# Kernel optimization log

Hardware: AMD Instinct MI355X
Metric: run time of the kernel (lower is better)

Reference implementation:

```python
import jax, jax.numpy as jnp
import numpy as np

# dims: batch, d_features(m), n_subsets, sub_size(k=ceil(m/n)), heads, d_k, d_v, conv kernel, d_out
B, M, N, K, H, DK, DV, KER, D = 512, 4096, 64, 64, 8, 32, 4, 3, 4096
DOUT_PER = D // N  # d_out_per_subset = 64
EPS_LN = 1e-5      # torch nn.LayerNorm default eps


def setup_inputs() -> dict:
    key = jax.random.key(0)
    ks = jax.random.split(key, 8)
    s = 0.02  # xavier-like scale
    return {
        "features": jax.random.normal(ks[0], (B, M), dtype=jnp.float32),
        # per-head permutation of the m feature indices (f_shuffle(m, h, seeds))
        "shuffled_index": jnp.argsort(jax.random.uniform(ks[1], (H, M)), axis=1).astype(jnp.int32),
        "gamma": jnp.ones((M,), jnp.float32),
        "beta": jnp.zeros((M,), jnp.float32),
        "W_q": (jax.random.normal(ks[2], (H * DK, K)) * s).astype(jnp.float32),   # Linear(k, h*d_k)
        "W_k": (jax.random.normal(ks[3], (H, DK, K)) * s).astype(jnp.float32),    # grouped Conv1d(h, h*d_k, kernel=k, stride=k)
        "W_v1": (jax.random.normal(ks[4], (H, DV, KER)) * s).astype(jnp.float32), # grouped Conv1d(h, h*d_v, kernel)
        "W_v2": (jax.random.normal(ks[5], (H, DV)) * s).astype(jnp.float32),      # grouped Conv1d(h*d_v, h, 1)
        "W_fc": (jax.random.normal(ks[6], (DOUT_PER, H * K)) * s).astype(jnp.float32),
    }


def reference(features, shuffled_index, gamma, beta, W_q, W_k, W_v1, W_v2, W_fc):
    b = features.shape[0]
    # LayerNorm over m (query path only)
    mu = features.mean(-1, keepdims=True)
    var = ((features - mu) ** 2).mean(-1, keepdims=True)
    q_in = (features - mu) / jnp.sqrt(var + EPS_LN) * gamma + beta

    # shuffled gather: [b, H, M]  (k*n == m here so k_pad/q_pad are no-ops)
    sf = features[:, shuffled_index]

    # query: [b, n, k] -> Linear(k, h*d_k) -> [b, H, N, DK]
    q = jnp.einsum('bnk,ek->bne', q_in.reshape(b, N, K), W_q)
    q = q.reshape(b, N, H, DK).transpose(0, 2, 1, 3)

    # key: grouped conv kernel=stride=k == per-subset contraction -> [b, H, DK, N]
    kf = sf.reshape(b, H, N, K)
    key_ = jnp.einsum('bhnk,hdk->bhdn', kf, W_k)

    # value: [b, N, H, K], right-pad by KER-1, depthwise conv -> relu -> 1x1 conv -> +residual
    v = kf.transpose(0, 2, 1, 3)  # [b, N, H, K]
    vp = jnp.pad(v, ((0, 0), (0, 0), (0, 0), (0, KER - 1)))
    win = jnp.stack([vp[..., t:t + K] for t in range(KER)], axis=-1)  # [b,N,H,K,KER]
    v1 = jnp.einsum('bnhpt,hdt->bnhdp', win, W_v1)
    v2 = jnp.einsum('bnhdp,hd->bnhp', jax.nn.relu(v1), W_v2)
    v = (v2 + v).transpose(0, 2, 1, 3)  # [b, H, N, K]

    # scaled dot-product attention, temperature = sqrt(m)
    attn = jax.nn.softmax(jnp.einsum('bhqd,bhdk->bhqk', q, key_) / jnp.sqrt(jnp.float32(M)), axis=-1)
    out = jnp.einsum('bhqk,bhks->bhqs', attn, v)           # [b, H, N, K]
    out = out.transpose(0, 2, 1, 3).reshape(b, N, H * K)   # [b, N, H*K]
    out = jnp.einsum('bnf,of->bno', out, W_fc).reshape(b, N * DOUT_PER)
    return out, attn.reshape(b * H, N, N)
```

## Files before the change

### kernel.cpp

```cpp
#include <hip/hip_runtime.h>

typedef __bf16 v8bf __attribute__((ext_vector_type(8)));
typedef __bf16 v4bf __attribute__((ext_vector_type(4)));
typedef __bf16 v2bf __attribute__((ext_vector_type(2)));
typedef float  v4f  __attribute__((ext_vector_type(4)));
typedef float  v2f  __attribute__((ext_vector_type(2)));
typedef unsigned long long u64;

namespace {

constexpr int kB = 512, kM = 4096, kH = 8;


__global__ __launch_bounds__(256) void k0_weights(
    const float* __restrict__ Wq, const float* __restrict__ Wk,
    const float* __restrict__ Wfc,
    __bf16* __restrict__ wq, __bf16* __restrict__ wk, __bf16* __restrict__ wfc,
    float* __restrict__ out) {
  int i = blockIdx.x * 256 + threadIdx.x;
  float4 z = make_float4(0.f, 0.f, 0.f, 0.f);
#pragma unroll
  for (int j = 0; j < 4; ++j) reinterpret_cast<float4*>(out)[i + j * 131072] = z;
  if (i < 16384) {
    int e = i >> 6, k = i & 63;
    int dst = ((e >> 4) * 2 + (k >> 5)) * 512 + (e & 15) * 32 + (k & 31);
    wq[dst] = (__bf16)(Wq[i] * 0.015625f);
  } else if (i < 32768) {
    int j = i - 16384;
    int e = j >> 6, k = j & 63;
    int dst = ((e >> 4) * 2 + (k >> 5)) * 512 + (e & 15) * 32 + (k & 31);
    wk[dst] = (__bf16)Wk[j];
  } else if (i < 65536) {
    int j = i - 32768;
    int o = j >> 9, f = j & 511;
    int dst = ((o >> 4) * 16 + (f >> 5)) * 512 + (o & 15) * 32 + (f & 31);
    wfc[dst] = (__bf16)Wfc[j];
  }
}

__global__ __launch_bounds__(256, 4) void k_fused(
    const float* __restrict__ feat, const int* __restrict__ sidx,
    const float* __restrict__ gamma, const float* __restrict__ beta,
    const __bf16* __restrict__ wq, const __bf16* __restrict__ wk,
    const float* __restrict__ Wv1, const float* __restrict__ Wv2,
    const __bf16* __restrict__ wfc, float* __restrict__ out) {
  __shared__ __align__(16) __bf16 smem[18432];
  __shared__ float red[4];
  __bf16* s_feat = smem;
  __bf16* s_kf   = smem + 4096;
  __bf16* s_K0   = smem + 8704;
  __bf16* s_K1   = smem + 11264;
  __bf16* s_vT   = smem + 13824;
  __bf16* s_qin  = smem + 4096;

  const int b = blockIdx.x, half = blockIdx.y, h0 = 4 * half;
  const int t = threadIdx.x, w = t >> 6, lane = t & 63;
  const int quad = lane >> 4, l16 = lane & 15;
  const int myrow = 16 * w + l16;

  const float4* frow4 = reinterpret_cast<const float4*>(feat + (size_t)b * kM);
  const float4* g4  = reinterpret_cast<const float4*>(gamma);
  const float4* be4 = reinterpret_cast<const float4*>(beta);
  float4 xs[4];
  float s = 0.f;
#pragma unroll
  for (int j = 0; j < 4; ++j) {
    xs[j] = frow4[t + j * 256];
    s += xs[j].x + xs[j].y + xs[j].z + xs[j].w;
  }
  int4 idxc[4];
  {
    const int* ibase = sidx + (size_t)h0 * kM + myrow * 64 + 8 * quad;
#pragma unroll
    for (int p = 0; p < 4; ++p)
      idxc[p] = *(const int4*)(ibase + 32 * (p >> 1) + 4 * (p & 1));
  }
#pragma unroll
  for (int o = 32; o > 0; o >>= 1) s += __shfl_xor(s, o);
  if (lane == 0) red[w] = s;
  __syncthreads();
  const float mu = (red[0] + red[1] + red[2] + red[3]) * (1.f / kM);
  float var_p = 0.f;
#pragma unroll
  for (int j = 0; j < 4; ++j) {
    float d0 = xs[j].x - mu, d1 = xs[j].y - mu, d2 = xs[j].z - mu, d3 = xs[j].w - mu;
    var_p += d0 * d0 + d1 * d1 + d2 * d2 + d3 * d3;
  }
#pragma unroll
  for (int o = 32; o > 0; o >>= 1) var_p += __shfl_xor(var_p, o);
  __syncthreads();
  if (lane == 0) red[w] = var_p;
  __syncthreads();
  const float var  = (red[0] + red[1] + red[2] + red[3]) * (1.f / kM);
  const float rstd = rsqrtf(var + 1e-5f);
#pragma unroll
  for (int j = 0; j < 4; ++j) {
    const int i4 = t + j * 256;
    float4 g = g4[i4], bt = be4[i4];
    v4bf fb, qb;
    fb[0] = (__bf16)xs[j].x; fb[1] = (__bf16)xs[j].y;
    fb[2] = (__bf16)xs[j].z; fb[3] = (__bf16)xs[j].w;
    qb[0] = (__bf16)((xs[j].x - mu) * rstd * g.x + bt.x);
    qb[1] = (__bf16)((xs[j].y - mu) * rstd * g.y + bt.y);
    qb[2] = (__bf16)((xs[j].z - mu) * rstd * g.z + bt.z);
    qb[3] = (__bf16)((xs[j].w - mu) * rstd * g.w + bt.w);
    *(v4bf*)(s_feat + 4 * i4) = fb;
    const int n = i4 >> 4, k = 4 * (t & 15);
    const int dst = ((n >> 4) * 2 + (k >> 5)) * 512 + (n & 15) * 32 + (k & 31);
    *(v4bf*)(s_qin + dst) = qb;
  }
  __syncthreads();

  const int qs = 16 * (2 * (quad & 1));
  v8bf aq[4];
  {
    v8bf aA0 = *(const v8bf*)(s_qin + (2 * w + 0) * 512 + l16 * 32 + 8 * quad);
    v8bf aA1 = *(const v8bf*)(s_qin + (2 * w + 1) * 512 + l16 * 32 + 8 * quad);
#pragma unroll
    for (int itq = 0; itq < 4; ++itq) {
      const int h = h0 + itq;
      v4f dq0 = {0.f, 0.f, 0.f, 0.f}, dq1 = {0.f, 0.f, 0.f, 0.f};
      v8bf b00 = *(const v8bf*)(wq + (size_t)(4 * h + 0) * 512 + l16 * 32 + 8 * quad);
      v8bf b01 = *(const v8bf*)(wq + (size_t)(4 * h + 1) * 512 + l16 * 32 + 8 * quad);
      v8bf b10 = *(const v8bf*)(wq + (size_t)(4 * h + 2) * 512 + l16 * 32 + 8 * quad);
      v8bf b11 = *(const v8bf*)(wq + (size_t)(4 * h + 3) * 512 + l16 * 32 + 8 * quad);
      dq0 = __builtin_amdgcn_mfma_f32_16x16x32_bf16(b00, aA0, dq0, 0, 0, 0);
      dq0 = __builtin_amdgcn_mfma_f32_16x16x32_bf16(b01, aA1, dq0, 0, 0, 0);
      dq1 = __builtin_amdgcn_mfma_f32_16x16x32_bf16(b10, aA0, dq1, 0, 0, 0);
      dq1 = __builtin_amdgcn_mfma_f32_16x16x32_bf16(b11, aA1, dq1, 0, 0, 0);
      v4bf p0, p1;
#pragma unroll
      for (int r = 0; r < 4; ++r) { p0[r] = (__bf16)dq0[r]; p1[r] = (__bf16)dq1[r]; }
      const u64 P0 = __builtin_bit_cast(u64, p0), P1 = __builtin_bit_cast(u64, p1);
      u64 s0p0 = __shfl(P0, l16 + qs),      s0p1 = __shfl(P1, l16 + qs);
      u64 s1p0 = __shfl(P0, l16 + qs + 16), s1p1 = __shfl(P1, l16 + qs + 16);
      v4bf lo = __builtin_bit_cast(v4bf, (quad >> 1) ? s0p1 : s0p0);
      v4bf hi = __builtin_bit_cast(v4bf, (quad >> 1) ? s1p1 : s1p0);
#pragma unroll
      for (int r = 0; r < 4; ++r) { aq[itq][r] = lo[r]; aq[itq][4 + r] = hi[r]; }
    }
  }

  v8bf g0, g1;
  g0[0] = s_feat[idxc[0].x]; g0[1] = s_feat[idxc[0].y];
  g0[2] = s_feat[idxc[0].z]; g0[3] = s_feat[idxc[0].w];
  g0[4] = s_feat[idxc[1].x]; g0[5] = s_feat[idxc[1].y];
  g0[6] = s_feat[idxc[1].z]; g0[7] = s_feat[idxc[1].w];
  g1[0] = s_feat[idxc[2].x]; g1[1] = s_feat[idxc[2].y];
  g1[2] = s_feat[idxc[2].z]; g1[3] = s_feat[idxc[2].w];
  g1[4] = s_feat[idxc[3].x]; g1[5] = s_feat[idxc[3].y];
  g1[6] = s_feat[idxc[3].z]; g1[7] = s_feat[idxc[3].w];
  __syncthreads();

  if (t < 64) { v8bf z = {}; *(v8bf*)(s_kf + t * 72 + 64) = z; }

  v4f acc[4] = {{0.f, 0.f, 0.f, 0.f}, {0.f, 0.f, 0.f, 0.f},
                {0.f, 0.f, 0.f, 0.f}, {0.f, 0.f, 0.f, 0.f}};
  v4bf Qprev[4];

  for (int it = 0; it < 4; ++it) {
    const int h = h0 + it;
    __bf16* s_K = (it & 1) ? s_K1 : s_K0;

    *(v8bf*)(s_kf + myrow * 72 + 8 * quad)      = g0;
    *(v8bf*)(s_kf + myrow * 72 + 32 + 8 * quad) = g1;
    {
      v4f dk0 = {0.f, 0.f, 0.f, 0.f}, dk1 = {0.f, 0.f, 0.f, 0.f};
      v8bf b00 = *(const v8bf*)(wk + (size_t)(4 * h + 0) * 512 + l16 * 32 + 8 * quad);
      v8bf b10 = *(const v8bf*)(wk + (size_t)(4 * h + 2) * 512 + l16 * 32 + 8 * quad);
      dk0 = __builtin_amdgcn_mfma_f32_16x16x32_bf16(b00, g0, dk0, 0, 0, 0);
      dk1 = __builtin_amdgcn_mfma_f32_16x16x32_bf16(b10, g0, dk1, 0, 0, 0);
      v8bf b01 = *(const v8bf*)(wk + (size_t)(4 * h + 1) * 512 + l16 * 32 + 8 * quad);
      v8bf b11 = *(const v8bf*)(wk + (size_t)(4 * h + 3) * 512 + l16 * 32 + 8 * quad);
      dk0 = __builtin_amdgcn_mfma_f32_16x16x32_bf16(b01, g1, dk0, 0, 0, 0);
      dk1 = __builtin_amdgcn_mfma_f32_16x16x32_bf16(b11, g1, dk1, 0, 0, 0);
      v4bf p0, p1;
#pragma unroll
      for (int r = 0; r < 4; ++r) { p0[r] = (__bf16)dk0[r]; p1[r] = (__bf16)dk1[r]; }
      *(v4bf*)(s_K + myrow * 40 + 4 * quad)      = p0;
      *(v4bf*)(s_K + myrow * 40 + 16 + 4 * quad) = p1;
    }

    if (it > 0) {
      const int hp = h - 1;
#pragma unroll
      for (int kt = 0; kt < 2; ++kt) {
        const u64 qA = __builtin_bit_cast(u64, Qprev[2 * kt]);
        const u64 qB = __builtin_bit_cast(u64, Qprev[2 * kt + 1]);
        u64 A0 = __shfl(qA, l16 + qs), A1 = __shfl(qA, l16 + qs + 16);
        u64 B0 = __shfl(qB, l16 + qs), B1 = __shfl(qB, l16 + qs + 16);
        v4bf lo = __builtin_bit_cast(v4bf, (quad >> 1) ? B0 : A0);
        v4bf hi = __builtin_bit_cast(v4bf, (quad >> 1) ? B1 : A1);
        v8bf a_fc;
#pragma unroll
        for (int r = 0; r < 4; ++r) { a_fc[r] = lo[r]; a_fc[4 + r] = hi[r]; }
#pragma unroll
        for (int nt = 0; nt < 4; ++nt) {
          v8bf bb = *(const v8bf*)(wfc + (size_t)(nt * 16 + hp * 2 + kt) * 512 + l16 * 32 + 8 * quad);
          acc[nt] = __builtin_amdgcn_mfma_f32_16x16x32_bf16(a_fc, bb, acc[nt], 0, 0, 0);
        }
      }
    }
    __syncthreads();

    {
      int4 ixn[4];
      if (it < 3) {
        const int* ibase = sidx + (size_t)(h + 1) * kM + myrow * 64 + 8 * quad;
#pragma unroll
        for (int p = 0; p < 4; ++p)
          ixn[p] = *(const int4*)(ibase + 32 * (p >> 1) + 4 * (p & 1));
      }
      const int n = lane, p0c = w * 16;
      float w1[4][3], w2[4];
#pragma unroll
      for (int d = 0; d < 4; ++d) {
#pragma unroll
        for (int c = 0; c < 3; ++c) w1[d][c] = Wv1[(h * 4 + d) * 3 + c];
        w2[d] = Wv2[h * 4 + d];
      }
      v8bf xa = *(const v8bf*)(s_kf + n * 72 + p0c);
      v8bf xb = *(const v8bf*)(s_kf + n * 72 + p0c + 8);
      v2bf xc = *(const v2bf*)(s_kf + n * 72 + p0c + 16);
      v2f x2[10];
#pragma unroll
      for (int j = 0; j < 8; ++j) { x2[j][0] = (float)xa[j]; x2[j][1] = (float)xb[j]; }
      x2[8][0] = (float)xb[0]; x2[8][1] = (float)xc[0];
      x2[9][0] = (float)xb[1]; x2[9][1] = (float)xc[1];
      const v2f z2 = {0.f, 0.f};
#pragma unroll
      for (int pp = 0; pp < 8; ++pp) {
        v2f a2 = x2[pp];
#pragma unroll
        for (int d = 0; d < 4; ++d) {
          v2f v1 = x2[pp] * w1[d][0] + x2[pp + 1] * w1[d][1] + x2[pp + 2] * w1[d][2];
          v1 = __builtin_elementwise_max(v1, z2);
          a2 = a2 + v1 * w2[d];
        }
        s_vT[(p0c + pp) * 72 + n]     = (__bf16)a2[0];
        s_vT[(p0c + pp + 8) * 72 + n] = (__bf16)a2[1];
      }
      if (it < 3) {
        g0[0] = s_feat[ixn[0].x]; g0[1] = s_feat[ixn[0].y];
        g0[2] = s_feat[ixn[0].z]; g0[3] = s_feat[ixn[0].w];
        g0[4] = s_feat[ixn[1].x]; g0[5] = s_feat[ixn[1].y];
        g0[6] = s_feat[ixn[1].z]; g0[7] = s_feat[ixn[1].w];
        g1[0] = s_feat[ixn[2].x]; g1[1] = s_feat[ixn[2].y];
        g1[2] = s_feat[ixn[2].z]; g1[3] = s_feat[ixn[2].w];
        g1[4] = s_feat[ixn[3].x]; g1[5] = s_feat[ixn[3].y];
        g1[6] = s_feat[ixn[3].z]; g1[7] = s_feat[ixn[3].w];
      }
    }
    __syncthreads();

    v4f sc[4];
#pragma unroll
    for (int nt = 0; nt < 4; ++nt) {
      v4f zz = {0.f, 0.f, 0.f, 0.f};
      v8bf bbK = *(const v8bf*)(s_K + (16 * nt + l16) * 40 + 8 * quad);
      sc[nt] = __builtin_amdgcn_mfma_f32_16x16x32_bf16(bbK, aq[it], zz, 0, 0, 0);
    }

    float mx = sc[0][0];
#pragma unroll
    for (int nt = 0; nt < 4; ++nt)
#pragma unroll
      for (int r = 0; r < 4; ++r) mx = fmaxf(mx, sc[nt][r]);
    mx = fmaxf(mx, __shfl_xor(mx, 16));
    mx = fmaxf(mx, __shfl_xor(mx, 32));
    float ssum = 0.f;
#pragma unroll
    for (int nt = 0; nt < 4; ++nt)
#pragma unroll
      for (int r = 0; r < 4; ++r) {
        float e = __expf(sc[nt][r] - mx);
        sc[nt][r] = e; ssum += e;
      }
    ssum += __shfl_xor(ssum, 16);
    ssum += __shfl_xor(ssum, 32);
    const float inv = 1.0f / ssum;
#pragma unroll
    for (int nt = 0; nt < 4; ++nt) sc[nt] *= inv;

    float* attn_out = out + (size_t)kB * kM + ((size_t)(b * kH + h)) * 4096;
#pragma unroll
    for (int nt = 0; nt < 4; ++nt)
      *(v4f*)(attn_out + myrow * 64 + 16 * nt + 4 * quad) = sc[nt];

    v4bf P[4];
#pragma unroll
    for (int nt = 0; nt < 4; ++nt)
#pragma unroll
      for (int r = 0; r < 4; ++r) P[nt][r] = (__bf16)sc[nt][r];

    v4f dOT[4] = {{0.f, 0.f, 0.f, 0.f}, {0.f, 0.f, 0.f, 0.f},
                  {0.f, 0.f, 0.f, 0.f}, {0.f, 0.f, 0.f, 0.f}};
#pragma unroll
    for (int kt = 0; kt < 2; ++kt) {
      const u64 pA = __builtin_bit_cast(u64, P[2 * kt]);
      const u64 pB = __builtin_bit_cast(u64, P[2 * kt + 1]);
      u64 A0 = __shfl(pA, l16 + qs), A1 = __shfl(pA, l16 + qs + 16);
      u64 B0 = __shfl(pB, l16 + qs), B1 = __shfl(pB, l16 + qs + 16);
      v4bf lo = __builtin_bit_cast(v4bf, (quad >> 1) ? B0 : A0);
      v4bf hi = __builtin_bit_cast(v4bf, (quad >> 1) ? B1 : A1);
      v8bf a_pv;
#pragma unroll
      for (int r = 0; r < 4; ++r) { a_pv[r] = lo[r]; a_pv[4 + r] = hi[r]; }
#pragma unroll
      for (int st = 0; st < 4; ++st) {
        v8bf bb = *(const v8bf*)(s_vT + (16 * st + l16) * 72 + 32 * kt + 8 * quad);
        dOT[st] = __builtin_amdgcn_mfma_f32_16x16x32_bf16(bb, a_pv, dOT[st], 0, 0, 0);
      }
    }
#pragma unroll
    for (int st = 0; st < 4; ++st)
#pragma unroll
      for (int r = 0; r < 4; ++r) Qprev[st][r] = (__bf16)dOT[st][r];
  }

  {
    const int hp = h0 + 3;
#pragma unroll
    for (int kt = 0; kt < 2; ++kt) {
      const u64 qA = __builtin_bit_cast(u64, Qprev[2 * kt]);
      const u64 qB = __builtin_bit_cast(u64, Qprev[2 * kt + 1]);
      u64 A0 = __shfl(qA, l16 + qs), A1 = __shfl(qA, l16 + qs + 16);
      u64 B0 = __shfl(qB, l16 + qs), B1 = __shfl(qB, l16 + qs + 16);
      v4bf lo = __builtin_bit_cast(v4bf, (quad >> 1) ? B0 : A0);
      v4bf hi = __builtin_bit_cast(v4bf, (quad >> 1) ? B1 : A1);
      v8bf a_fc;
#pragma unroll
      for (int r = 0; r < 4; ++r) { a_fc[r] = lo[r]; a_fc[4 + r] = hi[r]; }
#pragma unroll
      for (int nt = 0; nt < 4; ++nt) {
        v8bf bb = *(const v8bf*)(wfc + (size_t)(nt * 16 + hp * 2 + kt) * 512 + l16 * 32 + 8 * quad);
        acc[nt] = __builtin_amdgcn_mfma_f32_16x16x32_bf16(a_fc, bb, acc[nt], 0, 0, 0);
      }
    }
  }

  float* orow = out + (size_t)b * kM;
#pragma unroll
  for (int nt = 0; nt < 4; ++nt)
#pragma unroll
    for (int r = 0; r < 4; ++r)
      atomicAdd(&orow[(16 * w + 4 * quad + r) * 64 + 16 * nt + l16], acc[nt][r]);
}

}

extern "C" void kernel_launch(void* const* d_in, const int* in_sizes, int n_in,
                              void* d_out, int out_size, void* d_ws, size_t ws_size,
                              hipStream_t stream) {
  (void)in_sizes; (void)n_in; (void)out_size; (void)ws_size;
  const float* features = (const float*)d_in[0];
  const int*   sidx     = (const int*)d_in[1];
  const float* gamma    = (const float*)d_in[2];
  const float* beta     = (const float*)d_in[3];
  const float* Wq       = (const float*)d_in[4];
  const float* Wk       = (const float*)d_in[5];
  const float* Wv1      = (const float*)d_in[6];
  const float* Wv2      = (const float*)d_in[7];
  const float* Wfc      = (const float*)d_in[8];
  float* out = (float*)d_out;

  char* ws = (char*)d_ws;
  __bf16* ws_wq  = (__bf16*)(ws);
  __bf16* ws_wk  = (__bf16*)(ws + 32768);
  __bf16* ws_wfc = (__bf16*)(ws + 65536);

  hipLaunchKernelGGL(k0_weights, dim3(512), dim3(256), 0, stream,
                     Wq, Wk, Wfc, ws_wq, ws_wk, ws_wfc, out);
  hipLaunchKernelGGL(k_fused, dim3(kB, 2), dim3(256), 0, stream,
                     features, sidx, gamma, beta, ws_wq, ws_wk, Wv1, Wv2, ws_wfc, out);
}
```

Measured before the change: 130.9 us.

## Software-pipeline key staging across heads and fuse LayerNorm statistics into one pass

Computes the LayerNorm mean and mean-square in a single reduction, which removes the second reduction pass and two barriers. The per-head loop is restructured so the next head's gathered features and key projection are staged after the current head's scores and softmax. The current head's score MFMAs, softmax and attention store now run before the value convolution, and the W_fc tile loads are hoisted so they can overlap. The aim is to shorten the critical path and barrier stalls per head, at the cost of more live registers and a one-pass variance formula (E[x²]−μ²) that is less numerically robust.

```diff
diff --git a/kernel.cpp b/kernel.cpp
--- a/kernel.cpp
+++ b/kernel.cpp
@@ -45,7 +45,7 @@
     const float* __restrict__ Wv1, const float* __restrict__ Wv2,
     const __bf16* __restrict__ wfc, float* __restrict__ out) {
   __shared__ __align__(16) __bf16 smem[18432];
-  __shared__ float red[4];
+  __shared__ float red[8];
   __bf16* s_feat = smem;
   __bf16* s_kf   = smem + 4096;
   __bf16* s_K0   = smem + 8704;
@@ -62,11 +62,13 @@
   const float4* g4  = reinterpret_cast<const float4*>(gamma);
   const float4* be4 = reinterpret_cast<const float4*>(beta);
   float4 xs[4];
-  float s = 0.f;
+  float s = 0.f, s2 = 0.f;
 #pragma unroll
   for (int j = 0; j < 4; ++j) {
     xs[j] = frow4[t + j * 256];
-    s += xs[j].x + xs[j].y + xs[j].z + xs[j].w;
+    s  += xs[j].x + xs[j].y + xs[j].z + xs[j].w;
+    s2 += xs[j].x * xs[j].x + xs[j].y * xs[j].y
+        + xs[j].z * xs[j].z + xs[j].w * xs[j].w;
   }
   int4 idxc[4];
   {
@@ -76,23 +78,12 @@
       idxc[p] = *(const int4*)(ibase + 32 * (p >> 1) + 4 * (p & 1));
   }
 #pragma unroll
-  for (int o = 32; o > 0; o >>= 1) s += __shfl_xor(s, o);
-  if (lane == 0) red[w] = s;
+  for (int o = 32; o > 0; o >>= 1) { s += __shfl_xor(s, o); s2 += __shfl_xor(s2, o); }
+  if (lane == 0) { red[w] = s; red[4 + w] = s2; }
   __syncthreads();
   const float mu = (red[0] + red[1] + red[2] + red[3]) * (1.f / kM);
-  float var_p = 0.f;
-#pragma unroll
-  for (int j = 0; j < 4; ++j) {
-    float d0 = xs[j].x - mu, d1 = xs[j].y - mu, d2 = xs[j].z - mu, d3 = xs[j].w - mu;
-    var_p += d0 * d0 + d1 * d1 + d2 * d2 + d3 * d3;
-  }
-#pragma unroll
-  for (int o = 32; o > 0; o >>= 1) var_p += __shfl_xor(var_p, o);
-  __syncthreads();
-  if (lane == 0) red[w] = var_p;
-  __syncthreads();
-  const float var  = (red[0] + red[1] + red[2] + red[3]) * (1.f / kM);
-  const float rstd = rsqrtf(var + 1e-5f);
+  const float ms = (red[4] + red[5] + red[6] + red[7]) * (1.f / kM);
+  const float rstd = rsqrtf(ms - mu * mu + 1e-5f);
 #pragma unroll
   for (int j = 0; j < 4; ++j) {
     const int i4 = t + j * 256;
@@ -154,6 +145,27 @@
 
   if (t < 64) { v8bf z = {}; *(v8bf*)(s_kf + t * 72 + 64) = z; }
 
+  auto stage = [&](int hh, __bf16* sKdst) {
+    *(v8bf*)(s_kf + myrow * 72 + 8 * quad)      = g0;
+    *(v8bf*)(s_kf + myrow * 72 + 32 + 8 * quad) = g1;
+    v4f dk0 = {0.f, 0.f, 0.f, 0.f}, dk1 = {0.f, 0.f, 0.f, 0.f};
+    v8bf b00 = *(const v8bf*)(wk + (size_t)(4 * hh + 0) * 512 + l16 * 32 + 8 * quad);
+    v8bf b10 = *(const v8bf*)(wk + (size_t)(4 * hh + 2) * 512 + l16 * 32 + 8 * quad);
+    dk0 = __builtin_amdgcn_mfma_f32_16x16x32_bf16(b00, g0, dk0, 0, 0, 0);
+    dk1 = __builtin_amdgcn_mfma_f32_16x16x32_bf16(b10, g0, dk1, 0, 0, 0);
+    v8bf b01 = *(const v8bf*)(wk + (size_t)(4 * hh + 1) * 512 + l16 * 32 + 8 * quad);
+    v8bf b11 = *(const v8bf*)(wk + (size_t)(4 * hh + 3) * 512 + l16 * 32 + 8 * quad);
+    dk0 = __builtin_amdgcn_mfma_f32_16x16x32_bf16(b01, g1, dk0, 0, 0, 0);
+    dk1 = __builtin_amdgcn_mfma_f32_16x16x32_bf16(b11, g1, dk1, 0, 0, 0);
+    v4bf p0, p1;
+#pragma unroll
+    for (int r = 0; r < 4; ++r) { p0[r] = (__bf16)dk0[r]; p1[r] = (__bf16)dk1[r]; }
+    *(v4bf*)(sKdst + myrow * 40 + 4 * quad)      = p0;
+    *(v4bf*)(sKdst + myrow * 40 + 16 + 4 * quad) = p1;
+  };
+
+  stage(h0, s_K0);
+
   v4f acc[4] = {{0.f, 0.f, 0.f, 0.f}, {0.f, 0.f, 0.f, 0.f},
                 {0.f, 0.f, 0.f, 0.f}, {0.f, 0.f, 0.f, 0.f}};
   v4bf Qprev[4];
@@ -161,56 +173,66 @@
   for (int it = 0; it < 4; ++it) {
     const int h = h0 + it;
     __bf16* s_K = (it & 1) ? s_K1 : s_K0;
-
-    *(v8bf*)(s_kf + myrow * 72 + 8 * quad)      = g0;
-    *(v8bf*)(s_kf + myrow * 72 + 32 + 8 * quad) = g1;
-    {
-      v4f dk0 = {0.f, 0.f, 0.f, 0.f}, dk1 = {0.f, 0.f, 0.f, 0.f};
-      v8bf b00 = *(const v8bf*)(wk + (size_t)(4 * h + 0) * 512 + l16 * 32 + 8 * quad);
-      v8bf b10 = *(const v8bf*)(wk + (size_t)(4 * h + 2) * 512 + l16 * 32 + 8 * quad);
-      dk0 = __builtin_amdgcn_mfma_f32_16x16x32_bf16(b00, g0, dk0, 0, 0, 0);
-      dk1 = __builtin_amdgcn_mfma_f32_16x16x32_bf16(b10, g0, dk1, 0, 0, 0);
-      v8bf b01 = *(const v8bf*)(wk + (size_t)(4 * h + 1) * 512 + l16 * 32 + 8 * quad);
-      v8bf b11 = *(const v8bf*)(wk + (size_t)(4 * h + 3) * 512 + l16 * 32 + 8 * quad);
-      dk0 = __builtin_amdgcn_mfma_f32_16x16x32_bf16(b01, g1, dk0, 0, 0, 0);
-      dk1 = __builtin_amdgcn_mfma_f32_16x16x32_bf16(b11, g1, dk1, 0, 0, 0);
-      v4bf p0, p1;
-#pragma unroll
-      for (int r = 0; r < 4; ++r) { p0[r] = (__bf16)dk0[r]; p1[r] = (__bf16)dk1[r]; }
-      *(v4bf*)(s_K + myrow * 40 + 4 * quad)      = p0;
-      *(v4bf*)(s_K + myrow * 40 + 16 + 4 * quad) = p1;
-    }
-
+    __syncthreads();
+
+
+    int4 ixn[4];
+    if (it < 3) {
+      const int* ibase = sidx + (size_t)(h + 1) * kM + myrow * 64 + 8 * quad;
+#pragma unroll
+      for (int p = 0; p < 4; ++p)
+        ixn[p] = *(const int4*)(ibase + 32 * (p >> 1) + 4 * (p & 1));
+    }
+
+    v4f sc[4];
+#pragma unroll
+    for (int nt = 0; nt < 4; ++nt) {
+      v4f zz = {0.f, 0.f, 0.f, 0.f};
+      v8bf bbK = *(const v8bf*)(s_K + (16 * nt + l16) * 40 + 8 * quad);
+      sc[nt] = __builtin_amdgcn_mfma_f32_16x16x32_bf16(bbK, aq[it], zz, 0, 0, 0);
+    }
+
+    v8bf wf0[4];
     if (it > 0) {
       const int hp = h - 1;
 #pragma unroll
-      for (int kt = 0; kt < 2; ++kt) {
-        const u64 qA = __builtin_bit_cast(u64, Qprev[2 * kt]);
-        const u64 qB = __builtin_bit_cast(u64, Qprev[2 * kt + 1]);
-        u64 A0 = __shfl(qA, l16 + qs), A1 = __shfl(qA, l16 + qs + 16);
-        u64 B0 = __shfl(qB, l16 + qs), B1 = __shfl(qB, l16 + qs + 16);
-        v4bf lo = __builtin_bit_cast(v4bf, (quad >> 1) ? B0 : A0);
-        v4bf hi = __builtin_bit_cast(v4bf, (quad >> 1) ? B1 : A1);
-        v8bf a_fc;
-#pragma unroll
-        for (int r = 0; r < 4; ++r) { a_fc[r] = lo[r]; a_fc[4 + r] = hi[r]; }
-#pragma unroll
-        for (int nt = 0; nt < 4; ++nt) {
-          v8bf bb = *(const v8bf*)(wfc + (size_t)(nt * 16 + hp * 2 + kt) * 512 + l16 * 32 + 8 * quad);
-          acc[nt] = __builtin_amdgcn_mfma_f32_16x16x32_bf16(a_fc, bb, acc[nt], 0, 0, 0);
-        }
-      }
-    }
-    __syncthreads();
+      for (int nt = 0; nt < 4; ++nt)
+        wf0[nt] = *(const v8bf*)(wfc + (size_t)(nt * 16 + hp * 2) * 512 + l16 * 32 + 8 * quad);
+    }
+
+    float mx = sc[0][0];
+#pragma unroll
+    for (int nt = 0; nt < 4; ++nt)
+#pragma unroll
+      for (int r = 0; r < 4; ++r) mx = fmaxf(mx, sc[nt][r]);
+    mx = fmaxf(mx, __shfl_xor(mx, 16));
+    mx = fmaxf(mx, __shfl_xor(mx, 32));
+    float ssum = 0.f;
+#pragma unroll
+    for (int nt = 0; nt < 4; ++nt)
+#pragma unroll
+      for (int r = 0; r < 4; ++r) {
+        float e = __expf(sc[nt][r] - mx);
+        sc[nt][r] = e; ssum += e;
+      }
+    ssum += __shfl_xor(ssum, 16);
+    ssum += __shfl_xor(ssum, 32);
+    const float inv = 1.0f / ssum;
+#pragma unroll
+    for (int nt = 0; nt < 4; ++nt) sc[nt] *= inv;
+
+    float* attn_out = out + (size_t)kB * kM + ((size_t)(b * kH + h)) * 4096;
+#pragma unroll
+    for (int nt = 0; nt < 4; ++nt)
+      *(v4f*)(attn_out + myrow * 64 + 16 * nt + 4 * quad) = sc[nt];
+
+    v4bf P[4];
+#pragma unroll
+    for (int nt = 0; nt < 4; ++nt)
+#pragma unroll
+      for (int r = 0; r < 4; ++r) P[nt][r] = (__bf16)sc[nt][r];
 
     {
-      int4 ixn[4];
-      if (it < 3) {
-        const int* ibase = sidx + (size_t)(h + 1) * kM + myrow * 64 + 8 * quad;
-#pragma unroll
-        for (int p = 0; p < 4; ++p)
-          ixn[p] = *(const int4*)(ibase + 32 * (p >> 1) + 4 * (p & 1));
-      }
       const int n = lane, p0c = w * 16;
       float w1[4][3], w2[4];
 #pragma unroll
@@ -240,58 +262,55 @@
         s_vT[(p0c + pp) * 72 + n]     = (__bf16)a2[0];
         s_vT[(p0c + pp + 8) * 72 + n] = (__bf16)a2[1];
       }
-      if (it < 3) {
-        g0[0] = s_feat[ixn[0].x]; g0[1] = s_feat[ixn[0].y];
-        g0[2] = s_feat[ixn[0].z]; g0[3] = s_feat[ixn[0].w];
-        g0[4] = s_feat[ixn[1].x]; g0[5] = s_feat[ixn[1].y];
-        g0[6] = s_feat[ixn[1].z]; g0[7] = s_feat[ixn[1].w];
-        g1[0] = s_feat[ixn[2].x]; g1[1] = s_feat[ixn[2].y];
-        g1[2] = s_feat[ixn[2].z]; g1[3] = s_feat[ixn[2].w];
-        g1[4] = s_feat[ixn[3].x]; g1[5] = s_feat[ixn[3].y];
-        g1[6] = s_feat[ixn[3].z]; g1[7] = s_feat[ixn[3].w];
-      }
+    }
+
+    if (it > 0) {
+      const int hp = h - 1;
+      {
+        const u64 qA = __builtin_bit_cast(u64, Qprev[0]);
+        const u64 qB = __builtin_bit_cast(u64, Qprev[1]);
+        u64 A0 = __shfl(qA, l16 + qs), A1 = __shfl(qA, l16 + qs + 16);
+        u64 B0 = __shfl(qB, l16 + qs), B1 = __shfl(qB, l16 + qs + 16);
+        v4bf lo = __builtin_bit_cast(v4bf, (quad >> 1) ? B0 : A0);
+        v4bf hi = __builtin_bit_cast(v4bf, (quad >> 1) ? B1 : A1);
+        v8bf a_fc;
+#pragma unroll
+        for (int r = 0; r < 4; ++r) { a_fc[r] = lo[r]; a_fc[4 + r] = hi[r]; }
+#pragma unroll
+        for (int nt = 0; nt < 4; ++nt)
+          acc[nt] = __builtin_amdgcn_mfma_f32_16x16x32_bf16(a_fc, wf0[nt], acc[nt], 0, 0, 0);
+      }
+      {
+        const u64 qA = __builtin_bit_cast(u64, Qprev[2]);
+        const u64 qB = __builtin_bit_cast(u64, Qprev[3]);
+        u64 A0 = __shfl(qA, l16 + qs), A1 = __shfl(qA, l16 + qs + 16);
+        u64 B0 = __shfl(qB, l16 + qs), B1 = __shfl(qB, l16 + qs + 16);
+        v4bf lo = __builtin_bit_cast(v4bf, (quad >> 1) ? B0 : A0);
+        v4bf hi = __builtin_bit_cast(v4bf, (quad >> 1) ? B1 : A1);
+        v8bf a_fc;
+#pragma unroll
+        for (int r = 0; r < 4; ++r) { a_fc[r] = lo[r]; a_fc[4 + r] = hi[r]; }
+#pragma unroll
+        for (int nt = 0; nt < 4; ++nt) {
+          v8bf bb = *(const v8bf*)(wfc + (size_t)(nt * 16 + hp * 2 + 1) * 512 + l16 * 32 + 8 * quad);
+          acc[nt] = __builtin_amdgcn_mfma_f32_16x16x32_bf16(a_fc, bb, acc[nt], 0, 0, 0);
+        }
+      }
+    }
+
+    if (it < 3) {
+      g0[0] = s_feat[ixn[0].x]; g0[1] = s_feat[ixn[0].y];
+      g0[2] = s_feat[ixn[0].z]; g0[3] = s_feat[ixn[0].w];
+      g0[4] = s_feat[ixn[1].x]; g0[5] = s_feat[ixn[1].y];
+      g0[6] = s_feat[ixn[1].z]; g0[7] = s_feat[ixn[1].w];
+      g1[0] = s_feat[ixn[2].x]; g1[1] = s_feat[ixn[2].y];
+      g1[2] = s_feat[ixn[2].z]; g1[3] = s_feat[ixn[2].w];
+      g1[4] = s_feat[ixn[3].x]; g1[5] = s_feat[ixn[3].y];
+      g1[6] = s_feat[ixn[3].z]; g1[7] = s_feat[ixn[3].w];
     }
     __syncthreads();
 
-    v4f sc[4];
-#pragma unroll
-    for (int nt = 0; nt < 4; ++nt) {
-      v4f zz = {0.f, 0.f, 0.f, 0.f};
-      v8bf bbK = *(const v8bf*)(s_K + (16 * nt + l16) * 40 + 8 * quad);
-      sc[nt] = __builtin_amdgcn_mfma_f32_16x16x32_bf16(bbK, aq[it], zz, 0, 0, 0);
-    }
-
-    float mx = sc[0][0];
-#pragma unroll
-    for (int nt = 0; nt < 4; ++nt)
-#pragma unroll
-      for (int r = 0; r < 4; ++r) mx = fmaxf(mx, sc[nt][r]);
-    mx = fmaxf(mx, __shfl_xor(mx, 16));
-    mx = fmaxf(mx, __shfl_xor(mx, 32));
-    float ssum = 0.f;
-#pragma unroll
-    for (int nt = 0; nt < 4; ++nt)
-#pragma unroll
-      for (int r = 0; r < 4; ++r) {
-        float e = __expf(sc[nt][r] - mx);
-        sc[nt][r] = e; ssum += e;
-      }
-    ssum += __shfl_xor(ssum, 16);
-    ssum += __shfl_xor(ssum, 32);
-    const float inv = 1.0f / ssum;
-#pragma unroll
-    for (int nt = 0; nt < 4; ++nt) sc[nt] *= inv;
-
-    float* attn_out = out + (size_t)kB * kM + ((size_t)(b * kH + h)) * 4096;
-#pragma unroll
-    for (int nt = 0; nt < 4; ++nt)
-      *(v4f*)(attn_out + myrow * 64 + 16 * nt + 4 * quad) = sc[nt];
-
-    v4bf P[4];
-#pragma unroll
-    for (int nt = 0; nt < 4; ++nt)
-#pragma unroll
-      for (int r = 0; r < 4; ++r) P[nt][r] = (__bf16)sc[nt][r];
+    if (it < 3) stage(h + 1, (it & 1) ? s_K0 : s_K1);
 
     v4f dOT[4] = {{0.f, 0.f, 0.f, 0.f}, {0.f, 0.f, 0.f, 0.f},
                   {0.f, 0.f, 0.f, 0.f}, {0.f, 0.f, 0.f, 0.f}};
```

Result: no change. 129.2 us, median of 2 (-1.3%).
